# Kernel optimization log

Hardware: AMD Instinct MI355X
Metric: run time of the kernel (lower is better)

The kernel has to match this reference:

```python
import jax, jax.numpy as jnp
import numpy as np

B, N, C, H, FF = 8, 1024, 256, 8, 4
HD = C // H

def _lin(key, din, dout):
    kw, kb = jax.random.split(key)
    lim = 1.0 / np.sqrt(din)
    W = jax.random.uniform(kw, (din, dout), minval=-lim, maxval=lim, dtype=jnp.float32)
    b = jax.random.uniform(kb, (dout,), minval=-lim, maxval=lim, dtype=jnp.float32)
    return W, b

def setup_inputs():
    key = jax.random.key(0)
    k = jax.random.split(key, 8)
    h = jax.random.normal(k[0], (B, N, C), dtype=jnp.float32)
    coords = jax.random.normal(k[1], (B, N, 3), dtype=jnp.float32) * 3.0
    mask = jnp.broadcast_to(jnp.arange(N) < int(0.9 * N), (B, N))
    Wq, bq = _lin(k[2], C, C)
    Wk, bk = _lin(k[3], C, C)
    Wv, bv = _lin(k[4], C, C)
    Wo, bo = _lin(k[5], C, C)
    Wf1, bf1 = _lin(k[6], C, FF * C)
    Wf2, bf2 = _lin(k[7], FF * C, C)
    g1 = jnp.ones((C,), jnp.float32); b1 = jnp.zeros((C,), jnp.float32)
    g2 = jnp.ones((C,), jnp.float32); b2 = jnp.zeros((C,), jnp.float32)
    return dict(h=h, coords=coords, mask=mask, Wq=Wq, bq=bq, Wk=Wk, bk=bk,
                Wv=Wv, bv=bv, Wo=Wo, bo=bo, g1=g1, b1=b1, g2=g2, b2=b2,
                Wf1=Wf1, bf1=bf1, Wf2=Wf2, bf2=bf2)

def _layernorm(x, g, b, eps=1e-5):
    mu = x.mean(-1, keepdims=True)
    var = ((x - mu) ** 2).mean(-1, keepdims=True)
    return (x - mu) / jnp.sqrt(var + eps) * g + b

def _forward(h, coords, mask, Wq, bq, Wk, bk, Wv, bv, Wo, bo,
             g1, b1, g2, b2, Wf1, bf1, Wf2, bf2):
    B_, N_, C_ = h.shape
    scale = HD ** (-0.5)
    eps = 1e-8
    # pairwise squared distance, +inf for pairs touching a masked node
    pair_mask = mask[:, :, None] & mask[:, None, :]          # [B,N,N]
    diff = coords[:, :, None, :] - coords[:, None, :, :]      # [B,N,N,3]
    r2 = jnp.where(pair_mask, (diff * diff).sum(-1), jnp.inf)
    eye = jnp.eye(N_, dtype=bool)[None]                       # [1,N,N]
    valid = jnp.isfinite(r2)
    off = valid & ~eye
    r2_off = jnp.where(off, r2, 0.0)
    cnt_row = jnp.maximum(off.sum(-1, keepdims=True), 1)
    r2_row_mean = jnp.maximum(r2_off.sum(-1, keepdims=True) / cnt_row, 1e-4)
    r2_eff = jnp.where(eye, r2_row_mean, r2)
    r2_eff = jnp.clip(jnp.nan_to_num(r2_eff, posinf=1e8), 1e-6, 1e8)
    w_raw = jnp.where(valid, 1.0 / (r2_eff + eps), 0.0)
    w = w_raw / jnp.maximum(w_raw.sum(-1, keepdims=True), 1e-12)
    log_w = jnp.log(jnp.maximum(w, 1e-12))[:, None]           # [B,1,N,N]
    # attention
    x = _layernorm(h, g1, b1)
    q = (x @ Wq + bq).reshape(B_, N_, H, HD).transpose(0, 2, 1, 3)
    k = (x @ Wk + bk).reshape(B_, N_, H, HD).transpose(0, 2, 1, 3)
    v = (x @ Wv + bv).reshape(B_, N_, H, HD).transpose(0, 2, 1, 3)
    logits = jnp.einsum('bhnd,bhmd->bhnm', q, k) * scale + log_w
    mask_q = mask[:, None, :, None]
    mask_k = mask[:, None, None, :]
    pair_valid = valid[:, None] & mask_q & mask_k
    logits = jnp.where(pair_valid, logits, -1e9)
    logits = jnp.where(mask_q, logits, 0.0)
    attn = jax.nn.softmax(logits, axis=-1)
    attn = jnp.nan_to_num(attn, nan=0.0)
    out = jnp.einsum('bhnm,bhmd->bhnd', attn, v)
    out = out * mask_q.astype(out.dtype)
    out = out.transpose(0, 2, 1, 3).reshape(B_, N_, C_)
    out = out @ Wo + bo
    h = h + out
    y = _layernorm(h, g2, b2)
    y = jax.nn.gelu(y @ Wf1 + bf1, approximate=False) @ Wf2 + bf2
    return h + y

def reference(h, coords, mask, Wq, bq, Wk, bk, Wv, bv, Wo, bo,
              g1, b1, g2, b2, Wf1, bf1, Wf2, bf2):
    return _forward(h, coords, mask, Wq, bq, Wk, bk, Wv, bv, Wo, bo,
                    g1, b1, g2, b2, Wf1, bf1, Wf2, bf2)
```

## Files before the change

### kernel.cpp

```cpp
#include <hip/hip_runtime.h>
#include <math.h>

#define NN 1024
#define CC 256
#define HH 8
#define HDD 32
#define NV 921
#define WJ 960

typedef __bf16 bf16x8 __attribute__((ext_vector_type(8)));
typedef float f32x4 __attribute__((ext_vector_type(4)));
typedef float f32x16 __attribute__((ext_vector_type(16)));
typedef unsigned short u16x4 __attribute__((ext_vector_type(4)));
typedef unsigned short u16x8 __attribute__((ext_vector_type(8)));
typedef unsigned int u32x4 __attribute__((ext_vector_type(4)));

static __device__ __forceinline__ unsigned short f2b(float x) {
  union { __bf16 h; unsigned short u; } c; c.h = (__bf16)x; return c.u;
}
static __device__ __forceinline__ float b2f(unsigned short u) {
  union { float f; unsigned v; } c; c.v = ((unsigned)u) << 16; return c.f;
}

static __device__ __forceinline__ unsigned cvt_pk_bf16(float lo, float hi) {
  unsigned r;
  asm("v_cvt_pk_bf16_f32 %0, %1, %2" : "=v"(r) : "v"(lo), "v"(hi));
  return r;
}

static __device__ __forceinline__ float block_sum(float val, float* red) {
  #pragma unroll
  for (int off = 32; off > 0; off >>= 1) val += __shfl_xor(val, off);
  __syncthreads();
  if ((threadIdx.x & 63) == 0) red[threadIdx.x >> 6] = val;
  __syncthreads();
  return red[0] + red[1] + red[2] + red[3];
}

__global__ __launch_bounds__(256) void pair_stats_kernel(
    const float* __restrict__ coords, unsigned short* __restrict__ wP)
{
  __shared__ float csh[NN * 3];
  __shared__ float red[4];
  int base = blockIdx.x * 4;
  int b = base >> 10;
  int tid = threadIdx.x;
  const float* cb = coords + (size_t)b * NN * 3;
  for (int t = tid; t < NN * 3; t += 256) csh[t] = cb[t];
  __syncthreads();
  #pragma unroll
  for (int ii = 0; ii < 4; ii++) {
    int row = base + ii;
    int i = row & (NN - 1);
    unsigned short* wrow = wP + (size_t)row * WJ;
    if (i >= NV) {
      if (tid < 240) {
        ushort4 z = {0, 0, 0, 0};
        *(ushort4*)(wrow + tid * 4) = z;
      }
      continue;
    }
    float cix = csh[i*3+0], ciy = csh[i*3+1], ciz = csh[i*3+2];
    float r2loc[4];
    float part = 0.f;
    #pragma unroll
    for (int it = 0; it < 4; it++) {
      int j = tid + it * 256;
      float dx = cix - csh[j*3+0], dy = ciy - csh[j*3+1], dz = ciz - csh[j*3+2];
      float r2 = dx*dx + dy*dy + dz*dz;
      r2loc[it] = r2;
      if (j < NV && j != i) part += r2;
    }
    float s = block_sum(part, red);
    float rm = fmaxf(s * (1.0f / 920.0f), 1e-4f);
    float wpart = 0.f;
    #pragma unroll
    for (int it = 0; it < 4; it++) {
      int j = tid + it * 256;
      if (j < NV) {
        float r2e = (j == i) ? rm : r2loc[it];
        float r2c = fminf(fmaxf(r2e, 1e-6f), 1e8f);
        wpart += 1.0f / (r2c + 1e-8f);
      }
    }
    float sw = block_sum(wpart, red);
    float invsw = 1.0f / fmaxf(sw, 1e-12f);
    if (tid < 240) {
      ushort4 o;
      unsigned short* op = (unsigned short*)&o;
      #pragma unroll
      for (int e = 0; e < 4; e++) {
        int j = tid * 4 + e;
        float wv = 0.f;
        if (j < NV) {
          float dx = cix - csh[j*3+0], dy = ciy - csh[j*3+1], dz = ciz - csh[j*3+2];
          float r2 = dx*dx + dy*dy + dz*dz;
          float r2e = (j == i) ? rm : r2;
          float r2c = fminf(fmaxf(r2e, 1e-6f), 1e8f);
          wv = fmaxf((1.0f / (r2c + 1e-8f)) * invsw, 1e-12f);
        }
        op[e] = f2b(wv);
      }
      *(ushort4*)(wrow + tid * 4) = o;
    }
    __syncthreads();
  }
}

__global__ __launch_bounds__(256) void ln_bf16_kernel(
    const float* __restrict__ X, const float* __restrict__ g, const float* __restrict__ b,
    unsigned short* __restrict__ out)
{
  int w = threadIdx.x >> 6, lane = threadIdx.x & 63;
  int row = blockIdx.x * 4 + w;
  float4 x = *(const float4*)(X + (size_t)row * CC + lane * 4);
  float s = x.x + x.y + x.z + x.w;
  #pragma unroll
  for (int off = 1; off < 64; off <<= 1) s += __shfl_xor(s, off);
  float mu = s * (1.0f / 256.0f);
  float dx0 = x.x - mu, dx1 = x.y - mu, dx2 = x.z - mu, dx3 = x.w - mu;
  float s2 = dx0*dx0 + dx1*dx1 + dx2*dx2 + dx3*dx3;
  #pragma unroll
  for (int off = 1; off < 64; off <<= 1) s2 += __shfl_xor(s2, off);
  float rstd = 1.0f / sqrtf(s2 * (1.0f / 256.0f) + 1e-5f);
  float4 gv = *(const float4*)(g + lane * 4);
  float4 bv = *(const float4*)(b + lane * 4);
  ushort4 o;
  o.x = f2b(dx0 * rstd * gv.x + bv.x);
  o.y = f2b(dx1 * rstd * gv.y + bv.y);
  o.z = f2b(dx2 * rstd * gv.z + bv.z);
  o.w = f2b(dx3 * rstd * gv.w + bv.w);
  *(ushort4*)(out + (size_t)row * CC + lane * 4) = o;
}

__global__ __launch_bounds__(256) void wcvt_kernel(
    const float* __restrict__ Wq, const float* __restrict__ Wk, const float* __restrict__ Wv,
    const float* __restrict__ Wo, const float* __restrict__ Wf1, const float* __restrict__ Wf2,
    unsigned short* __restrict__ qkvT, unsigned short* __restrict__ woT,
    unsigned short* __restrict__ wf1T, unsigned short* __restrict__ wf2T,
    const float* __restrict__ bq, const float* __restrict__ bk, const float* __restrict__ bv,
    float* __restrict__ bqkv)
{
  int t = blockIdx.x;
  int tid = threadIdx.x;
  if (t == 768) {
    bqkv[tid] = bq[tid]; bqkv[256 + tid] = bk[tid]; bqkv[512 + tid] = bv[tid];
    return;
  }
  __shared__ float lds[32][33];
  const float* src; unsigned short* dst; int Kd, Nd, tk, tn;
  if (t < 256) {
    int wid = t >> 6, lt = t & 63;
    const float* srcs[4] = {Wq, Wk, Wv, Wo};
    unsigned short* dsts[4] = {qkvT, qkvT + 256 * 256, qkvT + 512 * 256, woT};
    src = srcs[wid]; dst = dsts[wid]; Kd = 256; Nd = 256; tk = lt >> 3; tn = lt & 7;
  } else if (t < 512) {
    int lt = t - 256;
    src = Wf1; dst = wf1T; Kd = 256; Nd = 1024; tk = lt >> 5; tn = lt & 31;
  } else {
    int lt = t - 512;
    src = Wf2; dst = wf2T; Kd = 1024; Nd = 256; tk = lt >> 3; tn = lt & 7;
  }
  int tx = tid & 31, ty = tid >> 5;
  #pragma unroll
  for (int it = 0; it < 4; it++) {
    int r = ty + it * 8;
    lds[r][tx] = src[(size_t)(tk * 32 + r) * Nd + tn * 32 + tx];
  }
  __syncthreads();
  #pragma unroll
  for (int it = 0; it < 4; it++) {
    int r = ty + it * 8;
    dst[(size_t)(tn * 32 + r) * Kd + tk * 32 + tx] = f2b(lds[tx][r]);
  }
}

template<int BM, int BN, bool GELU_EP, bool RES_ADD, int OUT_MODE>
__global__ __launch_bounds__(256) void gemm_mfma_kernel(
    const unsigned short* __restrict__ A, const unsigned short* __restrict__ BT,
    const float* __restrict__ bias, const float* __restrict__ res,
    void* __restrict__ out, float oscale, int M, int N, int K)
{
  constexpr int AFRAG = BM / 32;
  constexpr int NFRAG = BN / 32;
  constexpr int AIT = BM / 32, BIT = BN / 32;
  __shared__ unsigned short As[BM][72];
  __shared__ unsigned short Bs[BN][72];
  int tid = threadIdx.x;
  int w = tid >> 6, lane = tid & 63, lo = lane & 15, hi = lane >> 4;
  int wr = w >> 1, wc = w & 1;
  int bm = blockIdx.y * BM, bn = blockIdx.x * BN;
  f32x4 acc[AFRAG][NFRAG];
  #pragma unroll
  for (int a = 0; a < AFRAG; a++)
    #pragma unroll
    for (int nf = 0; nf < NFRAG; nf++) acc[a][nf] = (f32x4){0.f, 0.f, 0.f, 0.f};
  int arow = tid >> 3, acol = (tid & 7) * 8;
  u16x8 areg[AIT], breg[BIT];
  #pragma unroll
  for (int it = 0; it < AIT; it++)
    areg[it] = *(const u16x8*)(A + (size_t)(bm + arow + it * 32) * K + acol);
  #pragma unroll
  for (int it = 0; it < BIT; it++)
    breg[it] = *(const u16x8*)(BT + (size_t)(bn + arow + it * 32) * K + acol);
  for (int k0 = 0; k0 < K; k0 += 64) {
    __syncthreads();
    #pragma unroll
    for (int it = 0; it < AIT; it++) *(u16x8*)&As[arow + it * 32][acol] = areg[it];
    #pragma unroll
    for (int it = 0; it < BIT; it++) *(u16x8*)&Bs[arow + it * 32][acol] = breg[it];
    __syncthreads();
    if (k0 + 64 < K) {
      #pragma unroll
      for (int it = 0; it < AIT; it++)
        areg[it] = *(const u16x8*)(A + (size_t)(bm + arow + it * 32) * K + k0 + 64 + acol);
      #pragma unroll
      for (int it = 0; it < BIT; it++)
        breg[it] = *(const u16x8*)(BT + (size_t)(bn + arow + it * 32) * K + k0 + 64 + acol);
    }
    #pragma unroll
    for (int ks = 0; ks < 2; ks++) {
      bf16x8 bf[NFRAG];
      #pragma unroll
      for (int nf = 0; nf < NFRAG; nf++)
        bf[nf] = *(const bf16x8*)&Bs[wc * (BN / 2) + nf * 16 + lo][ks * 32 + hi * 8];
      #pragma unroll
      for (int a = 0; a < AFRAG; a++) {
        bf16x8 af = *(const bf16x8*)&As[wr * (BM / 2) + a * 16 + lo][ks * 32 + hi * 8];
        #pragma unroll
        for (int nf = 0; nf < NFRAG; nf++)
          acc[a][nf] = __builtin_amdgcn_mfma_f32_16x16x32_bf16(af, bf[nf], acc[a][nf], 0, 0, 0);
      }
    }
  }
  float biasv[NFRAG];
  #pragma unroll
  for (int nf = 0; nf < NFRAG; nf++)
    biasv[nf] = bias[bn + wc * (BN / 2) + nf * 16 + lo];
  #pragma unroll
  for (int a = 0; a < AFRAG; a++) {
    int gm0 = bm + wr * (BM / 2) + a * 16 + hi * 4;
    #pragma unroll
    for (int nf = 0; nf < NFRAG; nf++) {
      int gn = bn + wc * (BN / 2) + nf * 16 + lo;
      float vv[4];
      #pragma unroll
      for (int r = 0; r < 4; r++) {
        float v = acc[a][nf][r] + biasv[nf];
        if constexpr (RES_ADD) v += res[(size_t)(gm0 + r) * N + gn];
        if constexpr (GELU_EP) v = 0.5f * v * (1.0f + erff(v * 0.70710678118654752f));
        vv[r] = v;
      }
      if constexpr (OUT_MODE == 0) {
        float* of = (float*)out;
        #pragma unroll
        for (int r = 0; r < 4; r++) of[(size_t)(gm0 + r) * N + gn] = vv[r] * oscale;
      } else if constexpr (OUT_MODE == 1) {
        unsigned short* ob = (unsigned short*)out;
        #pragma unroll
        for (int r = 0; r < 4; r++) ob[(size_t)(gm0 + r) * N + gn] = f2b(vv[r] * oscale);
      } else {
        int cb = gn >> 8;
        int nl = gn & 255;
        unsigned short* qp = (unsigned short*)out;
        if (cb == 0) {
          #pragma unroll
          for (int r = 0; r < 4; r++) qp[(size_t)(gm0 + r) * 256 + nl] = f2b(vv[r] * oscale);
        } else if (cb == 1) {
          unsigned short* kp = qp + (size_t)M * 256;
          #pragma unroll
          for (int r = 0; r < 4; r++) kp[(size_t)(gm0 + r) * 256 + nl] = f2b(vv[r]);
        } else {
          unsigned short* vp = qp + (size_t)M * 512;
          int bidx = gm0 >> 10, tok = gm0 & 1023;
          ushort4 pk;
          pk.x = f2b(vv[0]); pk.y = f2b(vv[1]); pk.z = f2b(vv[2]); pk.w = f2b(vv[3]);
          *(ushort4*)&vp[(((size_t)(bidx * 256 + nl)) << 10) + tok] = pk;
        }
      }
    }
  }
}

__global__ __launch_bounds__(256, 2) void attn_mfma_kernel(
    const __bf16* __restrict__ q, const __bf16* __restrict__ k, const __bf16* __restrict__ vt,
    const unsigned short* __restrict__ wP, unsigned short* __restrict__ ao)
{
  __shared__ unsigned short Ktu[64][136];
  __shared__ unsigned short VTs[128][72];
  __shared__ unsigned short Wls[32][68];

  int tid = threadIdx.x;
  int w = tid >> 6;
  int lane = tid & 63;
  int il = lane & 31, hf = lane >> 5;
  int b = blockIdx.z, hg = blockIdx.y, it = blockIdx.x;
  int i0 = it * 32;
  int head = hg * 4 + w;
  int ig = i0 + il;

  const __bf16* qrow = q + ((size_t)(b * NN + ig)) * CC + head * HDD;
  bf16x8 qf0 = *(const bf16x8*)(qrow + hf * 8);
  bf16x8 qf1 = *(const bf16x8*)(qrow + 16 + hf * 8);

  f32x16 osum;
  #pragma unroll
  for (int r = 0; r < 16; r++) osum[r] = 0.f;
  float den = 0.f;

  int sjr = tid >> 4, scpos = (tid & 15) * 8;
  int vrow = tid >> 1, vcol = (tid & 1) * 32;
  int wrow = tid >> 3, wcol = (tid & 7) * 8;

  u16x8 kreg[4], vreg[4], wreg;

  if (i0 < NV) {
    {
      const __bf16* ksrc = k + ((size_t)(b * NN + sjr)) * CC + hg * 128 + scpos;
      #pragma unroll
      for (int rr = 0; rr < 4; rr++)
        kreg[rr] = *(const u16x8*)(ksrc + (size_t)(rr * 16) * CC);
      const __bf16* vsrc = vt + ((size_t)(b * CC + hg * 128 + vrow)) * NN + vcol;
      #pragma unroll
      for (int qq = 0; qq < 4; qq++)
        vreg[qq] = *(const u16x8*)(vsrc + qq * 8);
      wreg = *(const u16x8*)(wP + ((size_t)(b * NN + i0 + wrow)) * WJ + wcol);
    }
    for (int jt = 0; jt < 15; jt++) {
      __syncthreads();
      #pragma unroll
      for (int rr = 0; rr < 4; rr++)
        *(u16x8*)&Ktu[sjr + rr * 16][scpos] = kreg[rr];
      #pragma unroll
      for (int qq = 0; qq < 4; qq++)
        *(u16x8*)&VTs[vrow][vcol + qq * 8] = vreg[qq];
      *(u16x8*)&Wls[wrow][wcol] = wreg;
      __syncthreads();
      if (jt < 14) {
        int j0 = (jt + 1) * 64;
        const __bf16* ksrc = k + ((size_t)(b * NN + j0 + sjr)) * CC + hg * 128 + scpos;
        #pragma unroll
        for (int rr = 0; rr < 4; rr++)
          kreg[rr] = *(const u16x8*)(ksrc + (size_t)(rr * 16) * CC);
        const __bf16* vsrc = vt + ((size_t)(b * CC + hg * 128 + vrow)) * NN + j0 + vcol;
        #pragma unroll
        for (int qq = 0; qq < 4; qq++)
          vreg[qq] = *(const u16x8*)(vsrc + qq * 8);
        wreg = *(const u16x8*)(wP + ((size_t)(b * NN + i0 + wrow)) * WJ + j0 + wcol);
      }

      #pragma unroll
      for (int jblk = 0; jblk < 2; jblk++) {
        f32x16 s;
        #pragma unroll
        for (int r = 0; r < 16; r++) s[r] = 0.f;
        bf16x8 kf0 = *(const bf16x8*)&Ktu[jblk * 32 + il][w * 32 + hf * 8];
        bf16x8 kf1 = *(const bf16x8*)&Ktu[jblk * 32 + il][w * 32 + 16 + hf * 8];
        s = __builtin_amdgcn_mfma_f32_32x32x16_bf16(kf0, qf0, s, 0, 0, 0);
        s = __builtin_amdgcn_mfma_f32_32x32x16_bf16(kf1, qf1, s, 0, 0, 0);
        float p[16];
        #pragma unroll
        for (int qd = 0; qd < 4; qd++) {
          u16x4 w4 = *(const u16x4*)&Wls[il][jblk * 32 + qd * 8 + hf * 4];
          #pragma unroll
          for (int e = 0; e < 4; e++) {
            int r = qd * 4 + e;
            float pv = b2f(w4[e]) * __builtin_exp2f(s[r]);
            den += pv;
            p[r] = pv;
          }
        }
        #pragma unroll
        for (int kw = 0; kw < 2; kw++) {
          unsigned pk0 = cvt_pk_bf16(p[8 * kw + 0], p[8 * kw + 1]);
          unsigned pk1 = cvt_pk_bf16(p[8 * kw + 2], p[8 * kw + 3]);
          unsigned pk2 = cvt_pk_bf16(p[8 * kw + 4], p[8 * kw + 5]);
          unsigned pk3 = cvt_pk_bf16(p[8 * kw + 6], p[8 * kw + 7]);
          u32x4 frag;
#if __has_builtin(__builtin_amdgcn_permlane32_swap)
          {
            typedef unsigned uint2v __attribute__((ext_vector_type(2)));
            uint2v s02 = __builtin_amdgcn_permlane32_swap(pk0, pk2, false, false);
            uint2v s13 = __builtin_amdgcn_permlane32_swap(pk1, pk3, false, false);
            frag[0] = s02[0]; frag[1] = s13[0]; frag[2] = s02[1]; frag[3] = s13[1];
          }
#else
          {
            unsigned t0 = __shfl_xor((int)pk2, 32);
            unsigned t1 = __shfl_xor((int)pk3, 32);
            unsigned t2 = __shfl_xor((int)pk0, 32);
            unsigned t3 = __shfl_xor((int)pk1, 32);
            frag[0] = hf ? t0 : pk0;
            frag[1] = hf ? t1 : pk1;
            frag[2] = hf ? pk2 : t2;
            frag[3] = hf ? pk3 : t3;
          }
#endif
          bf16x8 pfrag;
          { union { u32x4 u; bf16x8 b; } cvt; cvt.u = frag; pfrag = cvt.b; }
          bf16x8 vfrag = *(const bf16x8*)&VTs[w * 32 + il][(jblk * 2 + kw) * 16 + hf * 8];
          osum = __builtin_amdgcn_mfma_f32_32x32x16_bf16(pfrag, vfrag, osum, 0, 0, 0);
        }
      }
    }
  }

  den += __shfl_xor(den, 32);
  float inv = (den > 0.f) ? 1.0f / den : 0.f;

  #pragma unroll
  for (int r = 0; r < 16; r++) {
    int ir = (r & 3) + 8 * (r >> 2) + 4 * hf;
    float sc = __shfl(inv, ir);
    ao[((size_t)(b * NN + i0 + ir)) * CC + head * HDD + il] = f2b(osum[r] * sc);
  }
}

extern "C" void kernel_launch(void* const* d_in, const int* in_sizes, int n_in,
                              void* d_out, int out_size, void* d_ws, size_t ws_size,
                              hipStream_t stream) {
  (void)in_sizes; (void)n_in; (void)out_size; (void)ws_size;
  const float* h      = (const float*)d_in[0];
  const float* coords = (const float*)d_in[1];
  const float* Wq  = (const float*)d_in[3];
  const float* bq  = (const float*)d_in[4];
  const float* Wk  = (const float*)d_in[5];
  const float* bk  = (const float*)d_in[6];
  const float* Wv  = (const float*)d_in[7];
  const float* bv  = (const float*)d_in[8];
  const float* Wo  = (const float*)d_in[9];
  const float* bo  = (const float*)d_in[10];
  const float* g1  = (const float*)d_in[11];
  const float* b1  = (const float*)d_in[12];
  const float* g2  = (const float*)d_in[13];
  const float* b2  = (const float*)d_in[14];
  const float* Wf1 = (const float*)d_in[15];
  const float* bf1 = (const float*)d_in[16];
  const float* Wf2 = (const float*)d_in[17];
  const float* bf2 = (const float*)d_in[18];

  const int M = 8 * NN;
  char* cur = (char*)d_ws;
  auto alloc = [&](size_t bytes) { char* p = cur; cur += (bytes + 255) & ~(size_t)255; return p; };
  unsigned short* wPb  = (unsigned short*)alloc((size_t)M * WJ * 2);
  unsigned short* qkvT = (unsigned short*)alloc(768 * 256 * 2);
  unsigned short* woT  = (unsigned short*)alloc(256 * 256 * 2);
  unsigned short* wf1T = (unsigned short*)alloc(1024 * 256 * 2);
  unsigned short* wf2T = (unsigned short*)alloc(256 * 1024 * 2);
  float* bqkv = (float*)alloc(768 * 4);
  unsigned short* x1b = (unsigned short*)alloc((size_t)M * CC * 2);
  unsigned short* x2b = (unsigned short*)alloc((size_t)M * CC * 2);
  unsigned short* qb  = (unsigned short*)alloc((size_t)M * CC * 2);
  unsigned short* kb_ = (unsigned short*)alloc((size_t)M * CC * 2);
  unsigned short* vtb = (unsigned short*)alloc((size_t)M * CC * 2);
  unsigned short* aob = (unsigned short*)alloc((size_t)M * CC * 2);
  unsigned short* y1b = qb;
  float* h1 = (float*)d_out;

  const float QSCALE2 = 0.25503486904512874f;

  pair_stats_kernel<<<M / 4, 256, 0, stream>>>(coords, wPb);
  wcvt_kernel<<<769, 256, 0, stream>>>(Wq, Wk, Wv, Wo, Wf1, Wf2,
                                       qkvT, woT, wf1T, wf2T, bq, bk, bv, bqkv);
  ln_bf16_kernel<<<M / 4, 256, 0, stream>>>(h, g1, b1, x1b);

  gemm_mfma_kernel<128, 128, false, false, 3><<<dim3(6, 64), 256, 0, stream>>>(
      x1b, qkvT, bqkv, nullptr, qb, QSCALE2, M, 768, 256);

  attn_mfma_kernel<<<dim3(32, 2, 8), 256, 0, stream>>>(
      (const __bf16*)qb, (const __bf16*)kb_, (const __bf16*)vtb, wPb, aob);

  gemm_mfma_kernel<64, 64, false, true, 0><<<dim3(4, 128), 256, 0, stream>>>(
      aob, woT, bo, h, h1, 1.0f, M, 256, 256);

  ln_bf16_kernel<<<M / 4, 256, 0, stream>>>(h1, g2, b2, x2b);

  gemm_mfma_kernel<128, 128, true, false, 1><<<dim3(8, 64), 256, 0, stream>>>(
      x2b, wf1T, bf1, nullptr, y1b, 1.0f, M, 1024, 256);

  gemm_mfma_kernel<64, 64, false, true, 0><<<dim3(4, 128), 256, 0, stream>>>(
      y1b, wf2T, bf2, h1, d_out, 1.0f, M, 256, 1024);
}
```

Baseline: 118.3 us.

## Share K/V tiles across two query sub-tiles per attention block and retune grids

The attention kernel now uses 512 threads, where two groups of four waves each handle a 32-row query sub-tile and share one K/V tile staged in LDS. This halves K/V global traffic per query row and halves the number of blocks. The pair-stats kernel now processes 8 rows per block, so each block reloads the coordinates less often. The QKV and FF1 GEMMs switch to 128x64 tiles with twice as many blocks. The trade-off is fewer attention blocks, 256 in total, which may underfill the GPU's CUs at one block per CU.

```diff
diff --git a/kernel.cpp b/kernel.cpp
--- a/kernel.cpp
+++ b/kernel.cpp
@@ -42,14 +42,14 @@
 {
   __shared__ float csh[NN * 3];
   __shared__ float red[4];
-  int base = blockIdx.x * 4;
+  int base = blockIdx.x * 8;
   int b = base >> 10;
   int tid = threadIdx.x;
   const float* cb = coords + (size_t)b * NN * 3;
   for (int t = tid; t < NN * 3; t += 256) csh[t] = cb[t];
   __syncthreads();
   #pragma unroll
-  for (int ii = 0; ii < 4; ii++) {
+  for (int ii = 0; ii < 8; ii++) {
     int row = base + ii;
     int i = row & (NN - 1);
     unsigned short* wrow = wP + (size_t)row * WJ;
@@ -282,22 +282,24 @@
   }
 }
 
-__global__ __launch_bounds__(256, 2) void attn_mfma_kernel(
+__global__ __launch_bounds__(512, 1) void attn_mfma_kernel(
     const __bf16* __restrict__ q, const __bf16* __restrict__ k, const __bf16* __restrict__ vt,
     const unsigned short* __restrict__ wP, unsigned short* __restrict__ ao)
 {
   __shared__ unsigned short Ktu[64][136];
   __shared__ unsigned short VTs[128][72];
-  __shared__ unsigned short Wls[32][68];
+  __shared__ unsigned short Wls[64][68];
 
   int tid = threadIdx.x;
-  int w = tid >> 6;
+  int w8 = tid >> 6;
+  int isub = w8 >> 2;
+  int wl = w8 & 3;
   int lane = tid & 63;
   int il = lane & 31, hf = lane >> 5;
   int b = blockIdx.z, hg = blockIdx.y, it = blockIdx.x;
-  int i0 = it * 32;
-  int head = hg * 4 + w;
-  int ig = i0 + il;
+  int i0 = it * 64;
+  int head = hg * 4 + wl;
+  int ig = i0 + isub * 32 + il;
 
   const __bf16* qrow = q + ((size_t)(b * NN + ig)) * CC + head * HDD;
   bf16x8 qf0 = *(const bf16x8*)(qrow + hf * 8);
@@ -308,45 +310,37 @@
   for (int r = 0; r < 16; r++) osum[r] = 0.f;
   float den = 0.f;
 
-  int sjr = tid >> 4, scpos = (tid & 15) * 8;
-  int vrow = tid >> 1, vcol = (tid & 1) * 32;
-  int wrow = tid >> 3, wcol = (tid & 7) * 8;
-
-  u16x8 kreg[4], vreg[4], wreg;
+  u16x8 kreg[2], vreg[2], wreg;
 
   if (i0 < NV) {
     {
-      const __bf16* ksrc = k + ((size_t)(b * NN + sjr)) * CC + hg * 128 + scpos;
-      #pragma unroll
-      for (int rr = 0; rr < 4; rr++)
-        kreg[rr] = *(const u16x8*)(ksrc + (size_t)(rr * 16) * CC);
-      const __bf16* vsrc = vt + ((size_t)(b * CC + hg * 128 + vrow)) * NN + vcol;
-      #pragma unroll
-      for (int qq = 0; qq < 4; qq++)
-        vreg[qq] = *(const u16x8*)(vsrc + qq * 8);
-      wreg = *(const u16x8*)(wP + ((size_t)(b * NN + i0 + wrow)) * WJ + wcol);
+      #pragma unroll
+      for (int i = 0; i < 2; i++) {
+        int c = tid + i * 512;
+        kreg[i] = *(const u16x8*)(k + ((size_t)(b * NN + (c >> 4))) * CC + hg * 128 + (c & 15) * 8);
+        vreg[i] = *(const u16x8*)(vt + ((size_t)(b * CC + hg * 128 + (c >> 3))) * NN + (c & 7) * 8);
+      }
+      wreg = *(const u16x8*)(wP + ((size_t)(b * NN + i0 + (tid >> 3))) * WJ + (tid & 7) * 8);
     }
     for (int jt = 0; jt < 15; jt++) {
       __syncthreads();
       #pragma unroll
-      for (int rr = 0; rr < 4; rr++)
-        *(u16x8*)&Ktu[sjr + rr * 16][scpos] = kreg[rr];
-      #pragma unroll
-      for (int qq = 0; qq < 4; qq++)
-        *(u16x8*)&VTs[vrow][vcol + qq * 8] = vreg[qq];
-      *(u16x8*)&Wls[wrow][wcol] = wreg;
+      for (int i = 0; i < 2; i++) {
+        int c = tid + i * 512;
+        *(u16x8*)&Ktu[c >> 4][(c & 15) * 8] = kreg[i];
+        *(u16x8*)&VTs[c >> 3][(c & 7) * 8] = vreg[i];
+      }
+      *(u16x8*)&Wls[tid >> 3][(tid & 7) * 8] = wreg;
       __syncthreads();
       if (jt < 14) {
         int j0 = (jt + 1) * 64;
-        const __bf16* ksrc = k + ((size_t)(b * NN + j0 + sjr)) * CC + hg * 128 + scpos;
-        #pragma unroll
-        for (int rr = 0; rr < 4; rr++)
-          kreg[rr] = *(const u16x8*)(ksrc + (size_t)(rr * 16) * CC);
-        const __bf16* vsrc = vt + ((size_t)(b * CC + hg * 128 + vrow)) * NN + j0 + vcol;
-        #pragma unroll
-        for (int qq = 0; qq < 4; qq++)
-          vreg[qq] = *(const u16x8*)(vsrc + qq * 8);
-        wreg = *(const u16x8*)(wP + ((size_t)(b * NN + i0 + wrow)) * WJ + j0 + wcol);
+        #pragma unroll
+        for (int i = 0; i < 2; i++) {
+          int c = tid + i * 512;
+          kreg[i] = *(const u16x8*)(k + ((size_t)(b * NN + j0 + (c >> 4))) * CC + hg * 128 + (c & 15) * 8);
+          vreg[i] = *(const u16x8*)(vt + ((size_t)(b * CC + hg * 128 + (c >> 3))) * NN + j0 + (c & 7) * 8);
+        }
+        wreg = *(const u16x8*)(wP + ((size_t)(b * NN + i0 + (tid >> 3))) * WJ + j0 + (tid & 7) * 8);
       }
 
       #pragma unroll
@@ -354,14 +348,14 @@
         f32x16 s;
         #pragma unroll
         for (int r = 0; r < 16; r++) s[r] = 0.f;
-        bf16x8 kf0 = *(const bf16x8*)&Ktu[jblk * 32 + il][w * 32 + hf * 8];
-        bf16x8 kf1 = *(const bf16x8*)&Ktu[jblk * 32 + il][w * 32 + 16 + hf * 8];
+        bf16x8 kf0 = *(const bf16x8*)&Ktu[jblk * 32 + il][wl * 32 + hf * 8];
+        bf16x8 kf1 = *(const bf16x8*)&Ktu[jblk * 32 + il][wl * 32 + 16 + hf * 8];
         s = __builtin_amdgcn_mfma_f32_32x32x16_bf16(kf0, qf0, s, 0, 0, 0);
         s = __builtin_amdgcn_mfma_f32_32x32x16_bf16(kf1, qf1, s, 0, 0, 0);
         float p[16];
         #pragma unroll
         for (int qd = 0; qd < 4; qd++) {
-          u16x4 w4 = *(const u16x4*)&Wls[il][jblk * 32 + qd * 8 + hf * 4];
+          u16x4 w4 = *(const u16x4*)&Wls[isub * 32 + il][jblk * 32 + qd * 8 + hf * 4];
           #pragma unroll
           for (int e = 0; e < 4; e++) {
             int r = qd * 4 + e;
@@ -398,7 +392,7 @@
 #endif
           bf16x8 pfrag;
           { union { u32x4 u; bf16x8 b; } cvt; cvt.u = frag; pfrag = cvt.b; }
-          bf16x8 vfrag = *(const bf16x8*)&VTs[w * 32 + il][(jblk * 2 + kw) * 16 + hf * 8];
+          bf16x8 vfrag = *(const bf16x8*)&VTs[wl * 32 + il][(jblk * 2 + kw) * 16 + hf * 8];
           osum = __builtin_amdgcn_mfma_f32_32x32x16_bf16(pfrag, vfrag, osum, 0, 0, 0);
         }
       }
@@ -412,7 +406,7 @@
   for (int r = 0; r < 16; r++) {
     int ir = (r & 3) + 8 * (r >> 2) + 4 * hf;
     float sc = __shfl(inv, ir);
-    ao[((size_t)(b * NN + i0 + ir)) * CC + head * HDD + il] = f2b(osum[r] * sc);
+    ao[((size_t)(b * NN + i0 + isub * 32 + ir)) * CC + head * HDD + il] = f2b(osum[r] * sc);
   }
 }
 
@@ -459,15 +453,15 @@
 
   const float QSCALE2 = 0.25503486904512874f;
 
-  pair_stats_kernel<<<M / 4, 256, 0, stream>>>(coords, wPb);
+  pair_stats_kernel<<<M / 8, 256, 0, stream>>>(coords, wPb);
   wcvt_kernel<<<769, 256, 0, stream>>>(Wq, Wk, Wv, Wo, Wf1, Wf2,
                                        qkvT, woT, wf1T, wf2T, bq, bk, bv, bqkv);
   ln_bf16_kernel<<<M / 4, 256, 0, stream>>>(h, g1, b1, x1b);
 
-  gemm_mfma_kernel<128, 128, false, false, 3><<<dim3(6, 64), 256, 0, stream>>>(
+  gemm_mfma_kernel<128, 64, false, false, 3><<<dim3(12, 64), 256, 0, stream>>>(
       x1b, qkvT, bqkv, nullptr, qb, QSCALE2, M, 768, 256);
 
-  attn_mfma_kernel<<<dim3(32, 2, 8), 256, 0, stream>>>(
+  attn_mfma_kernel<<<dim3(16, 2, 8), 512, 0, stream>>>(
       (const __bf16*)qb, (const __bf16*)kb_, (const __bf16*)vtb, wPb, aob);
 
   gemm_mfma_kernel<64, 64, false, true, 0><<<dim3(4, 128), 256, 0, stream>>>(
@@ -475,7 +469,7 @@
 
   ln_bf16_kernel<<<M / 4, 256, 0, stream>>>(h1, g2, b2, x2b);
 
-  gemm_mfma_kernel<128, 128, true, false, 1><<<dim3(8, 64), 256, 0, stream>>>(
+  gemm_mfma_kernel<128, 64, true, false, 1><<<dim3(16, 64), 256, 0, stream>>>(
       x2b, wf1T, bf1, nullptr, y1b, 1.0f, M, 1024, 256);
 
   gemm_mfma_kernel<64, 64, false, true, 0><<<dim3(4, 128), 256, 0, stream>>>(
```

Measured after the change: 117.7 us. Within noise of the previous version (-0.6%).
